# Kernel tuning notes

Hardware: AMD Instinct MI355X
Metric: run time of the kernel (lower is better)

## Reference

```python
import jax, jax.numpy as jnp
import numpy as np

B, D, H, W = 16, 512, 32, 32   # batch, input_dim, spatial
CD, K = 256, 8192              # codebook dim, num codes
COMMIT = 1.0


def setup_inputs() -> dict:
    key = jax.random.key(0)
    k0, k1, k2, k3 = jax.random.split(key, 4)
    x = jax.random.normal(k0, (B, D, H, W), dtype=jnp.float32)
    # project_in: Linear(D -> CD); project_out: Linear(CD -> D)
    W_in = jax.random.normal(k1, (CD, D), dtype=jnp.float32) * (1.0 / np.sqrt(D))
    b_in = jnp.zeros((CD,), dtype=jnp.float32)
    W_out = jax.random.normal(k2, (D, CD), dtype=jnp.float32) * (1.0 / np.sqrt(CD))
    b_out = jnp.zeros((D,), dtype=jnp.float32)
    codebook = jax.random.normal(k3, (K, CD), dtype=jnp.float32) * 0.05
    return {"x": x, "W_in": W_in, "b_in": b_in, "W_out": W_out,
            "b_out": b_out, "codebook": codebook}


def reference(x, W_in, b_in, W_out, b_out, codebook):
    b, d, h, w = x.shape
    # b d h w -> b (h w) d
    xt = x.reshape(b, d, h * w).transpose(0, 2, 1)
    z = xt @ W_in.T + b_in                              # [b, n, CD]
    # squared euclidean distances to all codes: ||z||^2 - 2 z.e + ||e||^2
    d2 = ((z * z).sum(-1, keepdims=True)
          - 2.0 * jnp.einsum('bnc,kc->bnk', z, codebook)
          + (codebook * codebook).sum(-1))              # [b, n, K]
    indices = jnp.argmin(d2, axis=-1)                   # [b, n] int
    q = codebook[indices]                               # [b, n, CD]
    # training branch: commitment loss + straight-through estimator
    commitment_loss = COMMIT * jnp.mean((jax.lax.stop_gradient(q) - z) ** 2)
    q_ste = z + jax.lax.stop_gradient(q - z)
    out = q_ste @ W_out.T + b_out                       # [b, n, d]
    out = out.transpose(0, 2, 1).reshape(b, d, h, w)    # b (h w) d -> b d h w
    return out, indices, commitment_loss
```

## Files before the change

### kernel.cpp

```cpp
#include <hip/hip_runtime.h>
#include <cfloat>
#include <cstdint>

#define B_      16
#define DIN     512
#define HW      1024
#define CDIM    256
#define KCODES  8192
#define NTOK    (B_ * HW)
#define OUT_ELEMS (B_ * DIN * HW)
#define NSTRIP  8
#define NPART2  16
#define CPS     (KCODES / NSTRIP)
#define MAXR    4096
#define RCHUNK  32
#define RBLOCKS 2048
#define LOSS_SCALE (1.0f / ((float)NTOK * (float)CDIM))
#define WSCALE      16.0f
#define INV_WS      0.0625f
#define INV_WS2     0.00390625f
#define NEG2_INV_WS (-0.125f)
#define BAND_SLACK  2e-3f
#define A_BYTES  131072
#define B_OFF    131072
#define EE_OFF   (131072 + 3 * 8192)
#define LDS_TOT  (EE_OFF + 4096)

typedef __attribute__((ext_vector_type(8))) _Float16 f16x8;
typedef __attribute__((ext_vector_type(4))) float f32x4;

static __device__ __forceinline__ short f2h(float f) {
  _Float16 h = (_Float16)f;
  return __builtin_bit_cast(short, h);
}
static __device__ __forceinline__ float h2f(short h) {
  return (float)__builtin_bit_cast(_Float16, h);
}

#define GLL16(gsrc, ldst)                                                      \
  __builtin_amdgcn_global_load_lds(                                           \
      (const __attribute__((address_space(1))) unsigned int*)(gsrc),          \
      (__attribute__((address_space(3))) unsigned int*)(ldst), 16, 0, 0)

#define PREP_CB_BLKS 2048
#define PREP_W_BLKS  128
#define PREP_X_BLKS  2048
__global__ __launch_bounds__(256) void k_prep(
    const float* __restrict__ cb, const float* __restrict__ Win,
    const float* __restrict__ Wout, const float* __restrict__ x,
    short* __restrict__ cb_hi, short* __restrict__ cb_lo, float* __restrict__ ee,
    short* __restrict__ wi_hi, short* __restrict__ wi_lo,
    short* __restrict__ wo_hi,
    short* __restrict__ xT_hi, short* __restrict__ xT_lo,
    float* __restrict__ loss, int* __restrict__ rcount, int* __restrict__ scal) {
  __shared__ float T[64][65];
  const int blk = blockIdx.x;
  const int tid = threadIdx.x;
  if (blk == 0 && tid < 2) {
    if (tid == 0) *loss = 0.0f; else *rcount = 0;
  }
  if (blk < PREP_CB_BLKS) {
    const int wid = (blk * 256 + tid) >> 6;
    const int lane = tid & 63;
    const float4 v = *(const float4*)(cb + (size_t)wid * CDIM + lane * 4);
    float s = v.x * v.x + v.y * v.y + v.z * v.z + v.w * v.w;
    const float sx = v.x * WSCALE, sy = v.y * WSCALE,
                sz = v.z * WSCALE, sw = v.w * WSCALE;
    short4 h, l;
    h.x = f2h(sx); l.x = f2h(sx - h2f(h.x));
    h.y = f2h(sy); l.y = f2h(sy - h2f(h.y));
    h.z = f2h(sz); l.z = f2h(sz - h2f(h.z));
    h.w = f2h(sw); l.w = f2h(sw - h2f(h.w));
    *(short4*)(cb_hi + (size_t)wid * CDIM + lane * 4) = h;
    *(short4*)(cb_lo + (size_t)wid * CDIM + lane * 4) = l;
    const float rx = v.x - h2f(h.x) * INV_WS;
    const float ry = v.y - h2f(h.y) * INV_WS;
    const float rz = v.z - h2f(h.z) * INV_WS;
    const float rw = v.w - h2f(h.w) * INV_WS;
    float rr = rx * rx + ry * ry + rz * rz + rw * rw;
#pragma unroll
    for (int off = 32; off > 0; off >>= 1) {
      s += __shfl_down(s, off, 64);
      rr += __shfl_down(rr, off, 64);
    }
    const int wv = tid >> 6;
    if (lane == 0) { ee[wid] = s; T[0][wv] = s; T[1][wv] = rr; }
    __syncthreads();
    if (tid == 0) {
      const float em = fmaxf(fmaxf(T[0][0], T[0][1]), fmaxf(T[0][2], T[0][3]));
      const float rm = fmaxf(fmaxf(T[1][0], T[1][1]), fmaxf(T[1][2], T[1][3]));
      atomicMax(scal + 0, __float_as_int(em));
      atomicMax(scal + 1, __float_as_int(rm));
    }
  } else if (blk < PREP_CB_BLKS + PREP_W_BLKS) {
    const int i = ((blk - PREP_CB_BLKS) * 256 + tid) * 4;
    {
      const float4 v = *(const float4*)(Win + i);
      const float sx = v.x * WSCALE, sy = v.y * WSCALE,
                  sz = v.z * WSCALE, sw = v.w * WSCALE;
      short4 h, l;
      h.x = f2h(sx); l.x = f2h(sx - h2f(h.x));
      h.y = f2h(sy); l.y = f2h(sy - h2f(h.y));
      h.z = f2h(sz); l.z = f2h(sz - h2f(h.z));
      h.w = f2h(sw); l.w = f2h(sw - h2f(h.w));
      *(short4*)(wi_hi + i) = h; *(short4*)(wi_lo + i) = l;
    }
    {
      const float4 v = *(const float4*)(Wout + i);
      short4 h;
      h.x = f2h(v.x * WSCALE);
      h.y = f2h(v.y * WSCALE);
      h.z = f2h(v.z * WSCALE);
      h.w = f2h(v.w * WSCALE);
      *(short4*)(wo_hi + i) = h;
    }
  } else {
    const int id = blk - PREP_CB_BLKS - PREP_W_BLKS;
    const int xb = id & 255, yb = id >> 8;
    const int b = xb >> 4;
    const int hw0 = (xb & 15) * 64;
    const int din0 = yb * 64;
    {
      const int r = tid >> 2;
      const int c = tid & 3;
      const float* src = x + ((size_t)b * DIN + din0 + r) * HW + hw0 + c * 16;
#pragma unroll
      for (int j = 0; j < 4; ++j) {
        const float4 v = *(const float4*)(src + j * 4);
        T[r][c * 16 + j * 4 + 0] = v.x;
        T[r][c * 16 + j * 4 + 1] = v.y;
        T[r][c * 16 + j * 4 + 2] = v.z;
        T[r][c * 16 + j * 4 + 3] = v.w;
      }
    }
    __syncthreads();
    {
      const int tt = tid & 63;
      const int c2 = tid >> 6;
      short h[16], l[16];
#pragma unroll
      for (int j = 0; j < 16; ++j) {
        const float f = T[c2 * 16 + j][tt];
        h[j] = f2h(f); l[j] = f2h(f - h2f(h[j]));
      }
      const size_t base = ((size_t)b * HW + hw0 + tt) * DIN + din0 + c2 * 16;
      *(f16x8*)(xT_hi + base)     = *(f16x8*)&h[0];
      *(f16x8*)(xT_hi + base + 8) = *(f16x8*)&h[8];
      *(f16x8*)(xT_lo + base)     = *(f16x8*)&l[0];
      *(f16x8*)(xT_lo + base + 8) = *(f16x8*)&l[8];
    }
  }
}

__global__ __launch_bounds__(256, 2) void k_proj_in_mfma(
    const short* __restrict__ xT_hi, const short* __restrict__ xT_lo,
    const short* __restrict__ wi_hi, const short* __restrict__ wi_lo,
    const float* __restrict__ bin,
    short* __restrict__ z_hi, short* __restrict__ z_lo) {
  __shared__ short lds_s[4 * 128 * 32];
  char* ldsc = (char*)lds_s;
  const int tid = threadIdx.x;
  const int w = tid >> 6, lane = tid & 63;
  const int quad = lane >> 4, l16 = lane & 15;
  const int wm = w >> 1, wn = w & 1;
  const int tok0 = blockIdx.x * 128;
  const int cd0 = blockIdx.y * 128;

  const int uA = (w << 6) + lane, uB = uA + 256;
  const int tA = uA >> 2, pA = uA & 3, qA = pA ^ ((tA >> 1) & 3);
  const int tB = uB >> 2, pB = uB & 3, qB = pB ^ ((tB >> 1) & 3);
  const int offA = tA * DIN + qA * 8;
  const int offB = tB * DIN + qB * 8;
  const short* gAh0 = xT_hi + (size_t)tok0 * DIN + offA;
  const short* gAh1 = xT_hi + (size_t)tok0 * DIN + offB;
  const short* gAl0 = xT_lo + (size_t)tok0 * DIN + offA;
  const short* gAl1 = xT_lo + (size_t)tok0 * DIN + offB;
  const short* gBh0 = wi_hi + (size_t)cd0 * DIN + offA;
  const short* gBh1 = wi_hi + (size_t)cd0 * DIN + offB;
  const short* gBl0 = wi_lo + (size_t)cd0 * DIN + offA;
  const short* gBl1 = wi_lo + (size_t)cd0 * DIN + offB;

  int aoffs[4], boffs[4];
#pragma unroll
  for (int mi = 0; mi < 4; ++mi) {
    const int t = wm * 64 + mi * 16 + l16;
    aoffs[mi] = t * 64 + (quad ^ ((t >> 1) & 3)) * 16;
  }
#pragma unroll
  for (int ni = 0; ni < 4; ++ni) {
    const int t = wn * 64 + ni * 16 + l16;
    boffs[ni] = 16384 + t * 64 + (quad ^ ((t >> 1) & 3)) * 16;
  }

  f32x4 acc[4][4];
#pragma unroll
  for (int mi = 0; mi < 4; ++mi)
#pragma unroll
    for (int ni = 0; ni < 4; ++ni) acc[mi][ni] = (f32x4){0.f, 0.f, 0.f, 0.f};

  for (int kb = 0; kb < DIN; kb += 32) {
    __syncthreads();
    GLL16(gAh0 + kb, ldsc + ((0 * 4 + w) << 10));
    GLL16(gAh1 + kb, ldsc + ((1 * 4 + w) << 10));
    GLL16(gAl0 + kb, ldsc + ((2 * 4 + w) << 10));
    GLL16(gAl1 + kb, ldsc + ((3 * 4 + w) << 10));
    GLL16(gBh0 + kb, ldsc + ((4 * 4 + w) << 10));
    GLL16(gBh1 + kb, ldsc + ((5 * 4 + w) << 10));
    GLL16(gBl0 + kb, ldsc + ((6 * 4 + w) << 10));
    GLL16(gBl1 + kb, ldsc + ((7 * 4 + w) << 10));
    __syncthreads();
    f16x8 ah[4], al[4], bh[4], bl[4];
#pragma unroll
    for (int mi = 0; mi < 4; ++mi) {
      ah[mi] = *(const f16x8*)(ldsc + aoffs[mi]);
      al[mi] = *(const f16x8*)(ldsc + 8192 + aoffs[mi]);
    }
#pragma unroll
    for (int ni = 0; ni < 4; ++ni) {
      bh[ni] = *(const f16x8*)(ldsc + boffs[ni]);
      bl[ni] = *(const f16x8*)(ldsc + 8192 + boffs[ni]);
    }
#pragma unroll
    for (int mi = 0; mi < 4; ++mi)
#pragma unroll
      for (int ni = 0; ni < 4; ++ni) {
        f32x4 c = acc[mi][ni];
        c = __builtin_amdgcn_mfma_f32_16x16x32_f16(ah[mi], bh[ni], c, 0, 0, 0);
        c = __builtin_amdgcn_mfma_f32_16x16x32_f16(ah[mi], bl[ni], c, 0, 0, 0);
        c = __builtin_amdgcn_mfma_f32_16x16x32_f16(al[mi], bh[ni], c, 0, 0, 0);
        acc[mi][ni] = c;
      }
  }
  float bv[4];
#pragma unroll
  for (int ni = 0; ni < 4; ++ni) bv[ni] = bin[cd0 + wn * 64 + ni * 16 + l16];
#pragma unroll
  for (int mi = 0; mi < 4; ++mi)
#pragma unroll
    for (int r = 0; r < 4; ++r) {
      const int t = tok0 + wm * 64 + mi * 16 + quad * 4 + r;
#pragma unroll
      for (int ni = 0; ni < 4; ++ni) {
        const int cd = cd0 + wn * 64 + ni * 16 + l16;
        const float o = acc[mi][ni][r] * INV_WS + bv[ni];
        const short h = f2h(o);
        z_hi[(size_t)t * CDIM + cd] = h;
        z_lo[(size_t)t * CDIM + cd] = f2h(o - h2f(h));
      }
    }
}

__global__ __launch_bounds__(512, 2) void k_argmin_mfma(
    const short* __restrict__ z_hi,
    const short* __restrict__ cb_hi,
    const float* __restrict__ ee,
    float* __restrict__ pm1v, int* __restrict__ pm1i, float* __restrict__ pm2v) {
  __shared__ short lds_s[LDS_TOT / 2];
  char* ldsc = (char*)lds_s;
  const int tid = threadIdx.x;
  const int w = tid >> 6, lane = tid & 63;
  const int quad = lane >> 4, l16 = lane & 15;
  const int wm = w >> 1, wn = w & 1;
  const int tok0 = blockIdx.x * 256;
  const int cbase = blockIdx.y * CPS;

#pragma unroll
  for (int r = 0; r < 16; ++r) {
    const int u = r * 512 + tid;
    const int c = u >> 10, t = (u >> 2) & 255, p = u & 3;
    const int q = p ^ ((t >> 1) & 3);
    GLL16(z_hi + (size_t)(tok0 + t) * CDIM + c * 32 + q * 8,
          ldsc + r * 8192 + (w << 10));
  }
  if (w < 4) {
    GLL16(ee + cbase + w * 256 + lane * 4, ldsc + EE_OFF + (w << 10));
  }
  const int crB = tid >> 2, pB = tid & 3;
  const int qB = pB ^ ((crB >> 1) & 3);
  const short* bsrc = cb_hi + (size_t)(cbase + crB) * CDIM + qB * 8;
  GLL16(bsrc, ldsc + B_OFF + (w << 10));
  GLL16(bsrc + 32, ldsc + B_OFF + 8192 + (w << 10));

  int aoffs[4], boffs[4];
#pragma unroll
  for (int mi = 0; mi < 4; ++mi) {
    const int t = wm * 64 + mi * 16 + l16;
    aoffs[mi] = t * 64 + (quad ^ ((t >> 1) & 3)) * 16;
  }
#pragma unroll
  for (int ni = 0; ni < 4; ++ni) {
    const int t = wn * 64 + ni * 16 + l16;
    boffs[ni] = t * 64 + (quad ^ ((t >> 1) & 3)) * 16;
  }
  const float* eelds = (const float*)(ldsc + EE_OFF);

  float mv[16], sv[16]; int mi_[16];
#pragma unroll
  for (int j = 0; j < 16; ++j) {
    mv[j] = FLT_MAX; sv[j] = FLT_MAX; mi_[j] = 0x7fffffff;
  }

  int cur = 0;
  for (int ct = 0; ct < 8; ++ct) {
    f32x4 acc[4][4];
#pragma unroll
    for (int mi = 0; mi < 4; ++mi)
#pragma unroll
      for (int ni = 0; ni < 4; ++ni) acc[mi][ni] = (f32x4){0.f, 0.f, 0.f, 0.f};

#pragma unroll
    for (int kbi = 0; kbi < 8; ++kbi) {
      const int s = ct * 8 + kbi;
      asm volatile("s_waitcnt vmcnt(1)" ::: "memory");
      __builtin_amdgcn_s_barrier();
      __builtin_amdgcn_sched_barrier(0);
      {
        const int s2 = (s + 2) & 63;
        const int nslot = cur + 2 - ((cur >= 1) ? 3 : 0);
        GLL16(bsrc + (size_t)(s2 >> 3) * 128 * CDIM + (s2 & 7) * 32,
              ldsc + B_OFF + (nslot << 13) + (w << 10));
      }
      const int abase = kbi << 14;
      const int bbase = B_OFF + (cur << 13);
      f16x8 ah[4], bh[4];
#pragma unroll
      for (int mi = 0; mi < 4; ++mi)
        ah[mi] = *(const f16x8*)(ldsc + abase + aoffs[mi]);
#pragma unroll
      for (int ni = 0; ni < 4; ++ni)
        bh[ni] = *(const f16x8*)(ldsc + bbase + boffs[ni]);
#pragma unroll
      for (int mi = 0; mi < 4; ++mi)
#pragma unroll
        for (int ni = 0; ni < 4; ++ni)
          acc[mi][ni] = __builtin_amdgcn_mfma_f32_16x16x32_f16(
              ah[mi], bh[ni], acc[mi][ni], 0, 0, 0);
      cur = (cur == 2) ? 0 : cur + 1;
    }
    const int ctile = cbase + ct * 128;
    float eev[4];
#pragma unroll
    for (int ni = 0; ni < 4; ++ni)
      eev[ni] = eelds[ct * 128 + wn * 64 + ni * 16 + l16];
    const int cb2 = ctile + wn * 64 + l16;
#pragma unroll
    for (int mi = 0; mi < 4; ++mi)
#pragma unroll
      for (int r = 0; r < 4; ++r) {
        const int j = mi * 4 + r;
#pragma unroll
        for (int ni = 0; ni < 4; ++ni) {
          const float s = fmaf(NEG2_INV_WS, acc[mi][ni][r], eev[ni]);
          sv[j] = fminf(sv[j], fmaxf(mv[j], s));
          if (s < mv[j]) { mv[j] = s; mi_[j] = cb2 + ni * 16; }
        }
      }
  }
#pragma unroll
  for (int off = 1; off < 16; off <<= 1) {
#pragma unroll
    for (int j = 0; j < 16; ++j) {
      const float ov = __shfl_xor(mv[j], off, 64);
      const int   oi = __shfl_xor(mi_[j], off, 64);
      const float os = __shfl_xor(sv[j], off, 64);
      const float snew = fminf(fminf(sv[j], os), fmaxf(mv[j], ov));
      if (ov < mv[j] || (ov == mv[j] && oi < mi_[j])) { mv[j] = ov; mi_[j] = oi; }
      sv[j] = snew;
    }
  }
  if (l16 == 0) {
    const int p = blockIdx.y * 2 + wn;
#pragma unroll
    for (int j = 0; j < 16; ++j) {
      const int mi = j >> 2, r = j & 3;
      const int t = tok0 + wm * 64 + mi * 16 + quad * 4 + r;
      const size_t o = (size_t)p * NTOK + t;
      pm1v[o] = mv[j]; pm1i[o] = mi_[j]; pm2v[o] = sv[j];
    }
  }
}

__global__ __launch_bounds__(256) void k_merge_rescue(
    const float* __restrict__ pm1v, const int* __restrict__ pm1i,
    const float* __restrict__ pm2v,
    const short* __restrict__ z_hi, const short* __restrict__ z_lo,
    const float* __restrict__ cb, const int* __restrict__ scal,
    int* __restrict__ idxi, float* __restrict__ idx_f,
    int* __restrict__ rlist, int* __restrict__ rcount,
    float* __restrict__ loss) {
  __shared__ float lpart[4];
  const int tid = threadIdx.x;
  const int wv = tid >> 6, lane = tid & 63;
  const int t = blockIdx.x * 4 + wv;
  float av = FLT_MAX, asv = FLT_MAX; int ai = 0x7fffffff;
  if (lane < NPART2) {
    const size_t po = (size_t)lane * NTOK + t;
    av = pm1v[po]; ai = pm1i[po]; asv = pm2v[po];
  }
  float m1v = av; int m1i = ai; float msv = asv;
#pragma unroll
  for (int off = 1; off < 64; off <<= 1) {
    const float ov = __shfl_xor(m1v, off, 64);
    const int   oi = __shfl_xor(m1i, off, 64);
    const float os = __shfl_xor(msv, off, 64);
    msv = fminf(msv, os);
    if (ov < m1v || (ov == m1v && oi < m1i)) { m1v = ov; m1i = oi; }
  }
  const short4 h4 = *(const short4*)(z_hi + (size_t)t * CDIM + lane * 4);
  const short4 l4 = *(const short4*)(z_lo + (size_t)t * CDIM + lane * 4);
  const float hx = h2f(h4.x), hy = h2f(h4.y), hz = h2f(h4.z), hw = h2f(h4.w);
  const float lx = h2f(l4.x), ly = h2f(l4.y), lz = h2f(l4.z), lw = h2f(l4.w);
  const float zx = hx + lx, zy = hy + ly, zz = hz + lz, zw = hw + lw;
  float zl2 = lx * lx + ly * ly + lz * lz + lw * lw;
  float zh2 = hx * hx + hy * hy + hz * hz + hw * hw;
#pragma unroll
  for (int off = 32; off > 0; off >>= 1) {
    zl2 += __shfl_xor(zl2, off, 64);
    zh2 += __shfl_xor(zh2, off, 64);
  }
  const float emax = sqrtf(__int_as_float(scal[0]));
  const float rmax = sqrtf(__int_as_float(scal[1]));
  const float band = 4.0f * (sqrtf(zl2) * emax + sqrtf(zh2) * rmax) + BAND_SLACK;
  const float thr = m1v + band;
  const unsigned long long ball = __ballot(av <= thr);
  const bool flag = (msv <= thr);
  int besti = m1i;
  if (__popcll(ball) > 1) {
    double bestv = 1e300; int bi = 0x7fffffff;
    unsigned long long bb = ball;
    while (bb) {
      const int c = __ffsll((long long)bb) - 1;
      bb &= bb - 1;
      const int ci = __shfl(ai, c, 64);
      const float4 ev = *(const float4*)(cb + (size_t)ci * CDIM + lane * 4);
      const double dx = (double)zx - (double)ev.x;
      const double dy = (double)zy - (double)ev.y;
      const double dz_ = (double)zz - (double)ev.z;
      const double dw = (double)zw - (double)ev.w;
      double d = dx * dx + dy * dy + dz_ * dz_ + dw * dw;
#pragma unroll
      for (int off = 32; off > 0; off >>= 1) d += __shfl_xor(d, off, 64);
      if (d < bestv || (d == bestv && ci < bi)) { bestv = d; bi = ci; }
    }
    besti = bi;
  }
  const float4 qv = *(const float4*)(cb + (size_t)besti * CDIM + lane * 4);
  const float dx = qv.x - zx;
  const float dy = qv.y - zy;
  const float dz_ = qv.z - zz;
  const float dw = qv.w - zw;
  float s = dx * dx + dy * dy + dz_ * dz_ + dw * dw;
#pragma unroll
  for (int off = 32; off > 0; off >>= 1) s += __shfl_down(s, off, 64);
  if (lane == 0) {
    idxi[t] = besti;
    idx_f[t] = (float)besti;
    lpart[wv] = s;
    if (flag) {
      const int pos = atomicAdd(rcount, 1);
      if (pos < MAXR) rlist[pos] = t;
    }
  }
  __syncthreads();
  if (tid == 0) {
    atomicAdd(loss, (lpart[0] + lpart[1] + lpart[2] + lpart[3]) * LOSS_SCALE);
  }
}

__global__ __launch_bounds__(256) void k_rescue_chunk(
    const short* __restrict__ z_hi, const short* __restrict__ z_lo,
    const float* __restrict__ cb,
    const int* __restrict__ rlist, const int* __restrict__ rcount,
    double* __restrict__ slotv, int* __restrict__ sloti) {
  const int cnt0 = *rcount;
  const int cnt = cnt0 < MAXR ? cnt0 : MAXR;
  const int li0 = blockIdx.x >> 5;
  const int chunk = blockIdx.x & (RCHUNK - 1);
  if (li0 >= cnt) return;
  __shared__ float zrow[CDIM];
  __shared__ double rv[256];
  __shared__ int ri[256];
  const int tid = threadIdx.x;
  for (int li = li0; li < cnt; li += RBLOCKS / RCHUNK) {
    const int t = rlist[li];
    zrow[tid] = h2f(z_hi[(size_t)t * CDIM + tid]) + h2f(z_lo[(size_t)t * CDIM + tid]);
    __syncthreads();
    const int k = chunk * 256 + tid;
    const float* e = cb + (size_t)k * CDIM;
    double s0 = 0.0, s1 = 0.0, s2 = 0.0, s3 = 0.0;
    for (int c = 0; c < CDIM; c += 4) {
      const float4 ev = *(const float4*)(e + c);
      const double d0 = (double)zrow[c]     - (double)ev.x;
      const double d1 = (double)zrow[c + 1] - (double)ev.y;
      const double d2 = (double)zrow[c + 2] - (double)ev.z;
      const double d3 = (double)zrow[c + 3] - (double)ev.w;
      s0 += d0 * d0; s1 += d1 * d1; s2 += d2 * d2; s3 += d3 * d3;
    }
    rv[tid] = (s0 + s1) + (s2 + s3);
    ri[tid] = k;
    __syncthreads();
    for (int off = 128; off > 0; off >>= 1) {
      if (tid < off) {
        if (rv[tid + off] < rv[tid] ||
            (rv[tid + off] == rv[tid] && ri[tid + off] < ri[tid])) {
          rv[tid] = rv[tid + off]; ri[tid] = ri[tid + off];
        }
      }
      __syncthreads();
    }
    if (tid == 0) {
      slotv[(size_t)li * RCHUNK + chunk] = rv[0];
      sloti[(size_t)li * RCHUNK + chunk] = ri[0];
    }
    __syncthreads();
  }
}

__global__ __launch_bounds__(256) void k_rescue_fin(
    const double* __restrict__ slotv, const int* __restrict__ sloti,
    const int* __restrict__ rlist, const int* __restrict__ rcount,
    const short* __restrict__ z_hi, const short* __restrict__ z_lo,
    const float* __restrict__ cb,
    int* __restrict__ idxi, float* __restrict__ idx_f, float* __restrict__ loss) {
  const int cnt0 = *rcount;
  const int cnt = cnt0 < MAXR ? cnt0 : MAXR;
  const int tid = threadIdx.x;
  const int wv = tid >> 6, lane = tid & 63;
  for (int li = wv; li < cnt; li += 4) {
    double bv = 1e300; int bx = 0x7fffffff;
    if (lane < RCHUNK) {
      bv = slotv[(size_t)li * RCHUNK + lane];
      bx = sloti[(size_t)li * RCHUNK + lane];
    }
#pragma unroll
    for (int off = 1; off < 32; off <<= 1) {
      const double ov = __shfl_xor(bv, off, 64);
      const int   oi = __shfl_xor(bx, off, 64);
      if (ov < bv || (ov == bv && oi < bx)) { bv = ov; bx = oi; }
    }
    const int newi = __shfl(bx, 0, 64);
    const int t = rlist[li];
    const int oldi = idxi[t];
    if (newi != oldi) {
      const short4 h4 = *(const short4*)(z_hi + (size_t)t * CDIM + lane * 4);
      const short4 l4 = *(const short4*)(z_lo + (size_t)t * CDIM + lane * 4);
      const float4 qn = *(const float4*)(cb + (size_t)newi * CDIM + lane * 4);
      const float4 qo = *(const float4*)(cb + (size_t)oldi * CDIM + lane * 4);
      const float zx = h2f(h4.x) + h2f(l4.x);
      const float zy = h2f(h4.y) + h2f(l4.y);
      const float zz = h2f(h4.z) + h2f(l4.z);
      const float zw = h2f(h4.w) + h2f(l4.w);
      float d = (qn.x - zx) * (qn.x - zx) - (qo.x - zx) * (qo.x - zx)
              + (qn.y - zy) * (qn.y - zy) - (qo.y - zy) * (qo.y - zy)
              + (qn.z - zz) * (qn.z - zz) - (qo.z - zz) * (qo.z - zz)
              + (qn.w - zw) * (qn.w - zw) - (qo.w - zw) * (qo.w - zw);
#pragma unroll
      for (int off = 32; off > 0; off >>= 1) d += __shfl_down(d, off, 64);
      if (lane == 0) {
        idxi[t] = newi;
        idx_f[t] = (float)newi;
        atomicAdd(loss, d * LOSS_SCALE);
      }
    }
  }
}

__global__ __launch_bounds__(256, 2) void k_proj_out_mfma(
    const short* __restrict__ wo_hi,
    const short* __restrict__ cb_hi, const short* __restrict__ cb_lo,
    const int* __restrict__ idxi, const float* __restrict__ bout,
    float* __restrict__ out) {
  __shared__ short lds_s[3 * 128 * 32];
  char* ldsc = (char*)lds_s;
  const int tid = threadIdx.x;
  const int w = tid >> 6, lane = tid & 63;
  const int quad = lane >> 4, l16 = lane & 15;
  const int wm = w >> 1, wn = w & 1;
  const int tok0 = blockIdx.x * 128;
  const int din0 = blockIdx.y * 128;

  const int uA = (w << 6) + lane, uB = uA + 256;
  const int tA = uA >> 2, pA = uA & 3, qA = pA ^ ((tA >> 1) & 3);
  const int tB = uB >> 2, pB = uB & 3, qB = pB ^ ((tB >> 1) & 3);
  const short* gAh0 = wo_hi + (size_t)(din0 + tA) * CDIM + qA * 8;
  const short* gAh1 = wo_hi + (size_t)(din0 + tB) * CDIM + qB * 8;
  const int iA = idxi[tok0 + tA];
  const int iB = idxi[tok0 + tB];
  const short* gBh0 = cb_hi + (size_t)iA * CDIM + qA * 8;
  const short* gBh1 = cb_hi + (size_t)iB * CDIM + qB * 8;
  const short* gBl0 = cb_lo + (size_t)iA * CDIM + qA * 8;
  const short* gBl1 = cb_lo + (size_t)iB * CDIM + qB * 8;

  int aoffs[4], boffs[4];
#pragma unroll
  for (int mi = 0; mi < 4; ++mi) {
    const int t = wm * 64 + mi * 16 + l16;
    aoffs[mi] = t * 64 + (quad ^ ((t >> 1) & 3)) * 16;
  }
#pragma unroll
  for (int ni = 0; ni < 4; ++ni) {
    const int t = wn * 64 + ni * 16 + l16;
    boffs[ni] = 8192 + t * 64 + (quad ^ ((t >> 1) & 3)) * 16;
  }

  f32x4 acc[4][4];
#pragma unroll
  for (int mi = 0; mi < 4; ++mi)
#pragma unroll
    for (int ni = 0; ni < 4; ++ni) acc[mi][ni] = (f32x4){0.f, 0.f, 0.f, 0.f};

  for (int kb = 0; kb < CDIM; kb += 32) {
    __syncthreads();
    GLL16(gAh0 + kb, ldsc + ((0 * 4 + w) << 10));
    GLL16(gAh1 + kb, ldsc + ((1 * 4 + w) << 10));
    GLL16(gBh0 + kb, ldsc + ((2 * 4 + w) << 10));
    GLL16(gBh1 + kb, ldsc + ((3 * 4 + w) << 10));
    GLL16(gBl0 + kb, ldsc + ((4 * 4 + w) << 10));
    GLL16(gBl1 + kb, ldsc + ((5 * 4 + w) << 10));
    __syncthreads();
    f16x8 ah[4], bh[4], bl[4];
#pragma unroll
    for (int mi = 0; mi < 4; ++mi)
      ah[mi] = *(const f16x8*)(ldsc + aoffs[mi]);
#pragma unroll
    for (int ni = 0; ni < 4; ++ni) {
      bh[ni] = *(const f16x8*)(ldsc + boffs[ni]);
      bl[ni] = *(const f16x8*)(ldsc + 8192 + boffs[ni]);
    }
#pragma unroll
    for (int mi = 0; mi < 4; ++mi)
#pragma unroll
      for (int ni = 0; ni < 4; ++ni) {
        f32x4 c = acc[mi][ni];
        c = __builtin_amdgcn_mfma_f32_16x16x32_f16(ah[mi], bh[ni], c, 0, 0, 0);
        c = __builtin_amdgcn_mfma_f32_16x16x32_f16(ah[mi], bl[ni], c, 0, 0, 0);
        acc[mi][ni] = c;
      }
  }
  const int b = tok0 >> 10;
  const int hwb = tok0 & (HW - 1);
  float* ob = out + (size_t)b * DIN * HW;
#pragma unroll
  for (int mi = 0; mi < 4; ++mi)
#pragma unroll
    for (int r = 0; r < 4; ++r) {
      const int din = din0 + wm * 64 + mi * 16 + quad * 4 + r;
      const float bb = bout[din];
#pragma unroll
      for (int ni = 0; ni < 4; ++ni) {
        const int hw = hwb + wn * 64 + ni * 16 + l16;
        ob[(size_t)din * HW + hw] = acc[mi][ni][r] * INV_WS2 + bb;
      }
    }
}

extern "C" void kernel_launch(void* const* d_in, const int* in_sizes, int n_in,
                              void* d_out, int out_size, void* d_ws, size_t ws_size,
                              hipStream_t stream) {
  const float* x    = (const float*)d_in[0];
  const float* Win  = (const float*)d_in[1];
  const float* bin  = (const float*)d_in[2];
  const float* Wout = (const float*)d_in[3];
  const float* bout = (const float*)d_in[4];
  const float* cb   = (const float*)d_in[5];

  float* out   = (float*)d_out;
  float* idx_f = out + OUT_ELEMS;
  float* loss  = out + OUT_ELEMS + NTOK;

  char* w = (char*)d_ws;
  size_t off = 0;
  short* z_hi  = (short*)(w + off); off += (size_t)NTOK * CDIM * 2;
  short* z_lo  = (short*)(w + off); off += (size_t)NTOK * CDIM * 2;
  short* cb_hi = (short*)(w + off); off += (size_t)KCODES * CDIM * 2;
  short* cb_lo = (short*)(w + off); off += (size_t)KCODES * CDIM * 2;
  short* xT_hi = (short*)(w + off); off += (size_t)NTOK * DIN * 2;
  short* xT_lo = (short*)(w + off); off += (size_t)NTOK * DIN * 2;
  short* wi_hi = (short*)(w + off); off += (size_t)CDIM * DIN * 2;
  short* wi_lo = (short*)(w + off); off += (size_t)CDIM * DIN * 2;
  short* wo_hi = (short*)(w + off); off += (size_t)DIN * CDIM * 2;
  float* ee    = (float*)(w + off); off += (size_t)KCODES * 4;
  int*   idxi  = (int*)(w + off);   off += (size_t)NTOK * 4;
  float* pm1v  = (float*)(w + off); off += (size_t)NPART2 * NTOK * 4;
  int*   pm1i  = (int*)(w + off);   off += (size_t)NPART2 * NTOK * 4;
  float* pm2v  = (float*)(w + off); off += (size_t)NPART2 * NTOK * 4;
  int*   rlist = (int*)(w + off);   off += (size_t)MAXR * 4;
  int*   rcount= (int*)(w + off);   off += 256;
  int*   scal  = (int*)(w + off);   off += 256;
  double* slotv= (double*)(w + off);off += (size_t)MAXR * RCHUNK * 8;
  int*   sloti = (int*)(w + off);   off += (size_t)MAXR * RCHUNK * 4;

  hipMemsetAsync(scal, 0, 8, stream);
  k_prep        <<<dim3(PREP_CB_BLKS + PREP_W_BLKS + PREP_X_BLKS),
                   dim3(256), 0, stream>>>(cb, Win, Wout, x, cb_hi, cb_lo, ee,
                                           wi_hi, wi_lo, wo_hi,
                                           xT_hi, xT_lo, loss, rcount, scal);
  k_proj_in_mfma<<<dim3(NTOK / 128, CDIM / 128), dim3(256), 0, stream>>>(
      xT_hi, xT_lo, wi_hi, wi_lo, bin, z_hi, z_lo);
  k_argmin_mfma <<<dim3(NTOK / 256, NSTRIP), dim3(512), 0, stream>>>(
      z_hi, cb_hi, ee, pm1v, pm1i, pm2v);
  k_merge_rescue<<<dim3(NTOK / 4), dim3(256), 0, stream>>>(
      pm1v, pm1i, pm2v, z_hi, z_lo, cb, scal, idxi, idx_f,
      rlist, rcount, loss);
  k_rescue_chunk<<<dim3(RBLOCKS), dim3(256), 0, stream>>>(
      z_hi, z_lo, cb, rlist, rcount, slotv, sloti);
  k_rescue_fin  <<<dim3(1), dim3(256), 0, stream>>>(
      slotv, sloti, rlist, rcount, z_hi, z_lo, cb, idxi, idx_f, loss);
  k_proj_out_mfma<<<dim3(NTOK / 128, DIN / 128), dim3(256), 0, stream>>>(
      wo_hi, cb_hi, cb_lo, idxi, bout, out);
}
```

Measured before the change: 436.3 us.

## Keep W_out tile resident in LDS and triple-buffer codebook gathers in proj_out

The output projection now uses 512-thread blocks covering 256 tokens by 128 output channels. The whole 128x256 fp16 W_out slice is loaded into LDS once up front. The gathered codebook hi/lo rows are streamed through a three-slot ring of async global-to-LDS loads, with vmcnt-based waits replacing the previous two full barriers per k-step. This is meant to hide gather latency behind MFMA work and cut redundant W_out reloads. The cost is about 160KB of LDS per block, which limits occupancy to roughly one block per CU, plus some wasted prefetch loads at the loop tail.

```diff
diff --git a/kernel.cpp b/kernel.cpp
--- a/kernel.cpp
+++ b/kernel.cpp
@@ -25,6 +25,8 @@
 #define B_OFF    131072
 #define EE_OFF   (131072 + 3 * 8192)
 #define LDS_TOT  (EE_OFF + 4096)
+#define PO_BOFF  65536
+#define PO_TOT   163840
 
 typedef __attribute__((ext_vector_type(8))) _Float16 f16x8;
 typedef __attribute__((ext_vector_type(4))) float f32x4;
@@ -565,31 +567,44 @@
   }
 }
 
-__global__ __launch_bounds__(256, 2) void k_proj_out_mfma(
+__global__ __launch_bounds__(512, 2) void k_proj_out_mfma(
     const short* __restrict__ wo_hi,
     const short* __restrict__ cb_hi, const short* __restrict__ cb_lo,
     const int* __restrict__ idxi, const float* __restrict__ bout,
     float* __restrict__ out) {
-  __shared__ short lds_s[3 * 128 * 32];
+  __shared__ short lds_s[PO_TOT / 2];
   char* ldsc = (char*)lds_s;
   const int tid = threadIdx.x;
   const int w = tid >> 6, lane = tid & 63;
   const int quad = lane >> 4, l16 = lane & 15;
-  const int wm = w >> 1, wn = w & 1;
-  const int tok0 = blockIdx.x * 128;
+  const int wm = w >> 2, wn = w & 3;
+  const int tok0 = blockIdx.x * 256;
   const int din0 = blockIdx.y * 128;
 
-  const int uA = (w << 6) + lane, uB = uA + 256;
-  const int tA = uA >> 2, pA = uA & 3, qA = pA ^ ((tA >> 1) & 3);
-  const int tB = uB >> 2, pB = uB & 3, qB = pB ^ ((tB >> 1) & 3);
-  const short* gAh0 = wo_hi + (size_t)(din0 + tA) * CDIM + qA * 8;
-  const short* gAh1 = wo_hi + (size_t)(din0 + tB) * CDIM + qB * 8;
-  const int iA = idxi[tok0 + tA];
-  const int iB = idxi[tok0 + tB];
-  const short* gBh0 = cb_hi + (size_t)iA * CDIM + qA * 8;
-  const short* gBh1 = cb_hi + (size_t)iB * CDIM + qB * 8;
-  const short* gBl0 = cb_lo + (size_t)iA * CDIM + qA * 8;
-  const short* gBl1 = cb_lo + (size_t)iB * CDIM + qB * 8;
+  const int tr = tid >> 2, p = tid & 3;
+  const int q = p ^ ((tr >> 1) & 3);
+  const int i0 = idxi[tok0 + tr];
+  const int i1 = idxi[tok0 + 128 + tr];
+  const short* s0h = cb_hi + (size_t)i0 * CDIM + q * 8;
+  const short* s1h = cb_hi + (size_t)i1 * CDIM + q * 8;
+  const short* s0l = cb_lo + (size_t)i0 * CDIM + q * 8;
+  const short* s1l = cb_lo + (size_t)i1 * CDIM + q * 8;
+
+#pragma unroll
+  for (int c = 0; c < 8; ++c)
+    GLL16(wo_hi + (size_t)(din0 + tr) * CDIM + c * 32 + q * 8,
+          ldsc + c * 8192 + (w << 10));
+
+#define PO_STAGE(s_, slot_)                                                    \
+  {                                                                            \
+    char* bb_ = ldsc + PO_BOFF + ((slot_) << 15);                              \
+    GLL16(s0h + (s_) * 32, bb_ + (w << 10));                                   \
+    GLL16(s1h + (s_) * 32, bb_ + 8192 + (w << 10));                            \
+    GLL16(s0l + (s_) * 32, bb_ + 16384 + (w << 10));                           \
+    GLL16(s1l + (s_) * 32, bb_ + 24576 + (w << 10));                           \
+  }
+  PO_STAGE(0, 0);
+  PO_STAGE(1, 1);
 
   int aoffs[4], boffs[4];
 #pragma unroll
@@ -600,7 +615,7 @@
 #pragma unroll
   for (int ni = 0; ni < 4; ++ni) {
     const int t = wn * 64 + ni * 16 + l16;
-    boffs[ni] = 8192 + t * 64 + (quad ^ ((t >> 1) & 3)) * 16;
+    boffs[ni] = t * 64 + (quad ^ ((t >> 1) & 3)) * 16;
   }
 
   f32x4 acc[4][4];
@@ -609,23 +624,27 @@
 #pragma unroll
     for (int ni = 0; ni < 4; ++ni) acc[mi][ni] = (f32x4){0.f, 0.f, 0.f, 0.f};
 
-  for (int kb = 0; kb < CDIM; kb += 32) {
-    __syncthreads();
-    GLL16(gAh0 + kb, ldsc + ((0 * 4 + w) << 10));
-    GLL16(gAh1 + kb, ldsc + ((1 * 4 + w) << 10));
-    GLL16(gBh0 + kb, ldsc + ((2 * 4 + w) << 10));
-    GLL16(gBh1 + kb, ldsc + ((3 * 4 + w) << 10));
-    GLL16(gBl0 + kb, ldsc + ((4 * 4 + w) << 10));
-    GLL16(gBl1 + kb, ldsc + ((5 * 4 + w) << 10));
-    __syncthreads();
+  int cur = 0;
+#pragma unroll
+  for (int s = 0; s < 8; ++s) {
+    asm volatile("s_waitcnt vmcnt(4)" ::: "memory");
+    __builtin_amdgcn_s_barrier();
+    __builtin_amdgcn_sched_barrier(0);
+    {
+      const int s2 = (s + 2) & 7;
+      const int nslot = cur + 2 - ((cur >= 1) ? 3 : 0);
+      PO_STAGE(s2, nslot);
+    }
+    const int abase = s << 13;
+    const int bbase = PO_BOFF + (cur << 15);
     f16x8 ah[4], bh[4], bl[4];
 #pragma unroll
     for (int mi = 0; mi < 4; ++mi)
-      ah[mi] = *(const f16x8*)(ldsc + aoffs[mi]);
+      ah[mi] = *(const f16x8*)(ldsc + abase + aoffs[mi]);
 #pragma unroll
     for (int ni = 0; ni < 4; ++ni) {
-      bh[ni] = *(const f16x8*)(ldsc + boffs[ni]);
-      bl[ni] = *(const f16x8*)(ldsc + 8192 + boffs[ni]);
+      bh[ni] = *(const f16x8*)(ldsc + bbase + boffs[ni]);
+      bl[ni] = *(const f16x8*)(ldsc + bbase + 16384 + boffs[ni]);
     }
 #pragma unroll
     for (int mi = 0; mi < 4; ++mi)
@@ -636,7 +655,10 @@
         c = __builtin_amdgcn_mfma_f32_16x16x32_f16(ah[mi], bl[ni], c, 0, 0, 0);
         acc[mi][ni] = c;
       }
-  }
+    cur = (cur == 2) ? 0 : cur + 1;
+  }
+#undef PO_STAGE
+
   const int b = tok0 >> 10;
   const int hwb = tok0 & (HW - 1);
   float* ob = out + (size_t)b * DIN * HW;
@@ -706,6 +728,6 @@
       z_hi, z_lo, cb, rlist, rcount, slotv, sloti);
   k_rescue_fin  <<<dim3(1), dim3(256), 0, stream>>>(
       slotv, sloti, rlist, rcount, z_hi, z_lo, cb, idxi, idx_f, loss);
-  k_proj_out_mfma<<<dim3(NTOK / 128, DIN / 128), dim3(256), 0, stream>>>(
+  k_proj_out_mfma<<<dim3(NTOK / 256, DIN / 128), dim3(512), 0, stream>>>(
       wo_hi, cb_hi, cb_lo, idxi, bout, out);
 }
```

After: 431.3 us. About the same (-1.2%).
